# Optimization experiments

Measured on AMD Instinct MI355X. Metric: run time of the kernel, lower is better.

The kernel has to match this reference:

```python
import jax, jax.numpy as jnp
import numpy as np

C = 256        # channel
C4 = C // 4    # q/k projection dim
B, NQ, NK = 2, 8192, 8192
BN_EPS = 1e-5


def setup_inputs() -> dict:
    key = jax.random.key(0)
    ks = jax.random.split(key, 8)
    q_tensor = jax.random.normal(ks[0], (B, NQ, C), dtype=jnp.float32)
    kv_tensor = jax.random.normal(ks[1], (B, NK, C), dtype=jnp.float32)
    # 1x1 Conv1d weights == linear layers over the channel dim
    wq = jax.random.normal(ks[2], (C4, C), dtype=jnp.float32) * 0.02
    wk = jax.random.normal(ks[3], (C4, C), dtype=jnp.float32) * 0.02
    wv = jax.random.normal(ks[4], (C, C), dtype=jnp.float32) * 0.02
    wt = jax.random.normal(ks[5], (C, C), dtype=jnp.float32) * 0.02
    bt = jnp.zeros((C,), dtype=jnp.float32)
    # BatchNorm1d (eval mode): affine params + running stats
    gamma = jax.random.uniform(ks[6], (C,), dtype=jnp.float32, minval=0.5, maxval=1.5)
    beta = jax.random.normal(ks[7], (C,), dtype=jnp.float32) * 0.1
    run_mean = jnp.zeros((C,), dtype=jnp.float32)
    run_var = jnp.ones((C,), dtype=jnp.float32)
    return {"q_tensor": q_tensor, "kv_tensor": kv_tensor, "wq": wq, "wk": wk,
            "wv": wv, "wt": wt, "bt": bt, "gamma": gamma, "beta": beta,
            "run_mean": run_mean, "run_var": run_var}


def reference(q_tensor, kv_tensor, wq, wk, wv, wt, bt, gamma, beta, run_mean, run_var):
    # 1x1 conv projections (channel-last form of Conv1d on permuted input)
    x_q = jnp.einsum('bnc,dc->bnd', q_tensor, wq)    # [B, NQ, C4]
    x_k = jnp.einsum('bnc,dc->bnd', kv_tensor, wk)   # [B, NK, C4]
    x_v = jnp.einsum('bnc,dc->bnd', kv_tensor, wv)   # [B, NK, C]
    # unscaled attention: matmul -> softmax -> matmul
    energy = jnp.einsum('bqd,bkd->bqk', x_q, x_k)    # [B, NQ, NK]
    attention = jax.nn.softmax(energy, axis=-1)
    x_r = jnp.einsum('bqk,bkc->bqc', attention, x_v)  # [B, NQ, C]
    # residual difference -> trans conv -> BN (eval) -> ReLU -> residual add
    res = q_tensor - x_r
    y = jnp.einsum('bnc,dc->bnd', res, wt) + bt
    y = (y - run_mean) * jax.lax.rsqrt(run_var + BN_EPS) * gamma + beta
    return jax.nn.relu(y) + q_tensor
```

## Files before the change

kernel.cpp:

```cpp
#include <hip/hip_runtime.h>
#include <hip/hip_bf16.h>

#define DEVINL __device__ __forceinline__

typedef short bf16x8 __attribute__((ext_vector_type(8)));
typedef float f32x4  __attribute__((ext_vector_type(4)));
typedef float f32x16 __attribute__((ext_vector_type(16)));
typedef unsigned int uint2v __attribute__((ext_vector_type(2)));

struct alignas(8) S4 { short x, y, z, w; };

DEVINL short f2bf(float f) {
  __hip_bfloat16 h = __float2bfloat16(f);
  short s; __builtin_memcpy(&s, &h, 2); return s;
}
DEVINL float bf2f(short s) {
  unsigned u = ((unsigned)(unsigned short)s) << 16;
  float f; __builtin_memcpy(&f, &u, 4); return f;
}

DEVINL f32x4 mfma16(bf16x8 a, bf16x8 b, f32x4 c) {
  return __builtin_amdgcn_mfma_f32_16x16x32_bf16(a, b, c, 0, 0, 0);
}
DEVINL f32x16 mfma32(bf16x8 a, bf16x8 b, f32x16 c) {
  return __builtin_amdgcn_mfma_f32_32x32x16_bf16(a, b, c, 0, 0, 0);
}

DEVINL void gld_lds16(const void* gptr, void* lptr) {
  __builtin_amdgcn_global_load_lds(
      (const __attribute__((address_space(1))) unsigned int*)gptr,
      (__attribute__((address_space(3))) unsigned int*)lptr, 16, 0, 0);
}

#define CC 256
#define C4 64
#define BB 2
#define NQ 8192
#define NK 8192
#define NROWS (BB * NQ)
#define LOG2E 1.44269504f

__global__ void k_setup(const float* __restrict__ wq, const float* __restrict__ wk,
                        const float* __restrict__ wv, const float* __restrict__ wt,
                        const float* __restrict__ bt, const float* __restrict__ gmm,
                        const float* __restrict__ bet, const float* __restrict__ rmean,
                        const float* __restrict__ rvar,
                        short* __restrict__ wqb, short* __restrict__ wkb,
                        short* __restrict__ wvb, short* __restrict__ wtb,
                        float* __restrict__ scale, float* __restrict__ bias) {
  int i = blockIdx.x * 256 + threadIdx.x;
  if (i < C4 * CC) { wqb[i] = f2bf(wq[i] * LOG2E); wkb[i] = f2bf(wk[i]); }
  if (i < CC * CC) { wvb[i] = f2bf(wv[i]); wtb[i] = f2bf(wt[i]); }
  if (i < CC) {
    float s = gmm[i] * rsqrtf(rvar[i] + 1e-5f);
    scale[i] = s;
    bias[i]  = (bt[i] - rmean[i]) * s + bet[i];
  }
}

__global__ __launch_bounds__(256)
void k_projqk(const float* __restrict__ q, const float* __restrict__ kv,
              const short* __restrict__ wqb, const short* __restrict__ wkb,
              short* __restrict__ xq, short* __restrict__ xk) {
  const float* A; const short* W; short* O;
  const bool swz = (blockIdx.y == 1);
  if (!swz) { A = q; W = wqb; O = xq; } else { A = kv; W = wkb; O = xk; }
  const int lane = threadIdx.x & 63, w = threadIdx.x >> 6;
  const int rowbase = blockIdx.x * 64 + w * 16;
  const int lr = lane & 15, lg = lane >> 4;
  f32x4 acc[4] = {};
#pragma unroll
  for (int kf = 0; kf < 8; ++kf) {
    const float* p = A + (size_t)(rowbase + lr) * CC + kf * 32 + lg * 8;
    float4 x0 = *(const float4*)p, x1 = *(const float4*)(p + 4);
    bf16x8 a;
    a[0] = f2bf(x0.x); a[1] = f2bf(x0.y); a[2] = f2bf(x0.z); a[3] = f2bf(x0.w);
    a[4] = f2bf(x1.x); a[5] = f2bf(x1.y); a[6] = f2bf(x1.z); a[7] = f2bf(x1.w);
#pragma unroll
    for (int nf = 0; nf < 4; ++nf) {
      bf16x8 b = *(const bf16x8*)(W + (size_t)(nf * 16 + lr) * CC + kf * 32 + lg * 8);
      acc[nf] = mfma16(a, b, acc[nf]);
    }
  }
#pragma unroll
  for (int nf = 0; nf < 4; ++nf)
#pragma unroll
    for (int r = 0; r < 4; ++r) {
      int row = rowbase + lg * 4 + r;
      int d = nf * 16 + lr;
      int off = swz ? ((((d >> 3) ^ (row & 7)) << 3) + (d & 7)) : d;
      O[(size_t)row * C4 + off] = f2bf(acc[nf][r]);
    }
}

__global__ __launch_bounds__(256)
void k_projv(const float* __restrict__ kv, const short* __restrict__ wvb,
             short* __restrict__ vt) {
  const int lane = threadIdx.x & 63, w = threadIdx.x >> 6;
  const int rowbase = blockIdx.x * 64 + w * 16;
  const int cb = blockIdx.y * 128;
  const int lr = lane & 15, lg = lane >> 4;
  f32x4 acc[8] = {};
#pragma unroll
  for (int kf = 0; kf < 8; ++kf) {
    const float* p = kv + (size_t)(rowbase + lr) * CC + kf * 32 + lg * 8;
    float4 x0 = *(const float4*)p, x1 = *(const float4*)(p + 4);
    bf16x8 a;
    a[0] = f2bf(x0.x); a[1] = f2bf(x0.y); a[2] = f2bf(x0.z); a[3] = f2bf(x0.w);
    a[4] = f2bf(x1.x); a[5] = f2bf(x1.y); a[6] = f2bf(x1.z); a[7] = f2bf(x1.w);
#pragma unroll
    for (int nf = 0; nf < 8; ++nf) {
      bf16x8 b = *(const bf16x8*)(wvb + (size_t)(cb + nf * 16 + lr) * CC + kf * 32 + lg * 8);
      acc[nf] = mfma16(a, b, acc[nf]);
    }
  }
  {
    int row = rowbase + lg * 4;
    int bidx = row >> 13, kib = row & 8191;
    int tile = kib >> 6, kk = kib & 63;
#pragma unroll
    for (int nf = 0; nf < 8; ++nf) {
      int c = cb + nf * 16 + lr;
      S4 st;
      st.x = f2bf(acc[nf][0]); st.y = f2bf(acc[nf][1]);
      st.z = f2bf(acc[nf][2]); st.w = f2bf(acc[nf][3]);
      int off = (((kk >> 3) ^ (c & 7)) << 3) + (kk & 7);
      *(S4*)(vt + (((size_t)bidx * 128 + tile) * CC + c) * 64 + off) = st;
    }
  }
}

__global__ __launch_bounds__(256, 2)
void k_attn(const short* __restrict__ xq, const short* __restrict__ xk,
            const short* __restrict__ vt, float* __restrict__ xr,
            short* __restrict__ po, float* __restrict__ pl, int nsplit) {
  __shared__ char Lds[81920];
  const int tid = threadIdx.x;
  const int ln = tid & 63, w = tid >> 6;
  const int qcol = ln & 31, hi = ln >> 5;
  const int b = blockIdx.y, qt = blockIdx.x, kz = blockIdx.z;
  const int kpb = (NK / 64) / nsplit;
  const int kt0 = kz * kpb, kt1 = kt0 + kpb;

  bf16x8 qb[4];
  {
    const short* qrow = xq + (size_t)(b * NQ + qt * 128 + w * 32 + qcol) * C4;
#pragma unroll
    for (int ds = 0; ds < 4; ++ds)
      qb[ds] = *(const bf16x8*)(qrow + ds * 16 + hi * 8);
  }
  f32x16 o[8] = {};
  float lsum = 0.f;

  const char* kgbase = (const char*)(xk + (size_t)b * NK * C4);
  const char* vgbase = (const char*)(vt + (size_t)b * 128 * 16384);

  auto stage = [&](int kt, char* base) {
    const char* ks = kgbase + (size_t)kt * 8192;
    const char* vs = vgbase + (size_t)kt * 32768;
#pragma unroll
    for (int i = 0; i < 2; ++i)
      gld_lds16(ks + (w * 2 + i) * 1024 + ln * 16, base + (w * 2 + i) * 1024);
#pragma unroll
    for (int i = 0; i < 8; ++i)
      gld_lds16(vs + (w * 8 + i) * 1024 + ln * 16, base + 8192 + (w * 8 + i) * 1024);
  };

  f32x16 s[2];
  bf16x8 pb[4];

  stage(kt0, Lds);
#pragma unroll 1
  for (int t = kt0; t < kt1; ++t) {
    char* cur = Lds + ((t - kt0) & 1) * 40960;
    char* nxt = Lds + ((~(t - kt0)) & 1) * 40960;
    asm volatile("s_waitcnt vmcnt(0)" ::: "memory");
    __builtin_amdgcn_s_barrier();
    __builtin_amdgcn_sched_barrier(0);
    if (t + 1 < kt1) stage(t + 1, nxt);
    s[0] = (f32x16)0.f; s[1] = (f32x16)0.f;
    __builtin_amdgcn_s_setprio(1);
#pragma unroll
    for (int kb = 0; kb < 2; ++kb) {
      int key = kb * 32 + qcol;
#pragma unroll
      for (int ds = 0; ds < 4; ++ds) {
        int cc = ds * 2 + hi;
        bf16x8 ka = *(const bf16x8*)(cur + key * 128 + ((cc ^ (key & 7)) << 4));
        s[kb] = mfma32(ka, qb[ds], s[kb]);
      }
    }
    __builtin_amdgcn_s_setprio(0);
    float rs = 0.f;
#pragma unroll
    for (int kb = 0; kb < 2; ++kb)
#pragma unroll
      for (int r = 0; r < 16; ++r) {
        float p = __builtin_amdgcn_exp2f(s[kb][r]);
        s[kb][r] = p; rs += p;
      }
    rs += __shfl_xor(rs, 32);
    lsum += rs;
#pragma unroll
    for (int kb = 0; kb < 2; ++kb) {
      unsigned wv[4], uv[4];
#pragma unroll
      for (int j = 0; j < 4; ++j) {
        asm("v_cvt_pk_bf16_f32 %0, %1, %2"
            : "=v"(wv[j]) : "v"(s[kb][4 * j + 0]), "v"(s[kb][4 * j + 1]));
        asm("v_cvt_pk_bf16_f32 %0, %1, %2"
            : "=v"(uv[j]) : "v"(s[kb][4 * j + 2]), "v"(s[kb][4 * j + 3]));
      }
#pragma unroll
      for (int jj = 0; jj < 2; ++jj) {
        uint2v rw = __builtin_amdgcn_permlane32_swap(wv[2 * jj], wv[2 * jj + 1], false, false);
        uint2v ru = __builtin_amdgcn_permlane32_swap(uv[2 * jj], uv[2 * jj + 1], false, false);
        unsigned tmp[4] = { rw[0], ru[0], rw[1], ru[1] };
        bf16x8 t2; __builtin_memcpy(&t2, tmp, 16);
        pb[kb * 2 + jj] = t2;
      }
    }
    __builtin_amdgcn_s_setprio(1);
#pragma unroll
    for (int cb = 0; cb < 8; ++cb) {
      int c = cb * 32 + qcol;
#pragma unroll
      for (int ks = 0; ks < 4; ++ks) {
        int cc = ks * 2 + hi;
        bf16x8 va = *(const bf16x8*)(cur + 8192 + c * 128 + ((cc ^ (c & 7)) << 4));
        o[cb] = mfma32(va, pb[ks], o[cb]);
      }
    }
    __builtin_amdgcn_s_setprio(0);
  }
  __builtin_amdgcn_s_barrier();

  char* tb = Lds + w * 4096;
  const size_t rb = (size_t)b * NQ + qt * 128 + w * 32;
  if (nsplit == 1) {
    float inv = 1.f / lsum;
#pragma unroll
    for (int cb = 0; cb < 8; ++cb) {
#pragma unroll
      for (int j = 0; j < 4; ++j) {
        f32x4 v;
        v[0] = o[cb][4 * j + 0] * inv; v[1] = o[cb][4 * j + 1] * inv;
        v[2] = o[cb][4 * j + 2] * inv; v[3] = o[cb][4 * j + 3] * inv;
        *(f32x4*)(tb + qcol * 128 + (((2 * j + hi) ^ (qcol & 7)) << 4)) = v;
      }
#pragma unroll
      for (int jr = 0; jr < 4; ++jr) {
        int qr = jr * 8 + (ln >> 3), cc = ln & 7;
        f32x4 v = *(const f32x4*)(tb + qr * 128 + ((cc ^ (qr & 7)) << 4));
        *(f32x4*)(xr + (rb + qr) * CC + cb * 32 + cc * 4) = v;
      }
    }
  } else {
#pragma unroll
    for (int cb = 0; cb < 8; ++cb) {
#pragma unroll
      for (int j = 0; j < 4; ++j) {
        f32x4 v;
        v[0] = o[cb][4 * j + 0]; v[1] = o[cb][4 * j + 1];
        v[2] = o[cb][4 * j + 2]; v[3] = o[cb][4 * j + 3];
        *(f32x4*)(tb + qcol * 128 + (((2 * j + hi) ^ (qcol & 7)) << 4)) = v;
      }
#pragma unroll
      for (int jr = 0; jr < 4; ++jr) {
        int qr = jr * 8 + (ln >> 3), cc = ln & 7;
        f32x4 v = *(const f32x4*)(tb + qr * 128 + ((cc ^ (qr & 7)) << 4));
        S4 sv; sv.x = f2bf(v[0]); sv.y = f2bf(v[1]); sv.z = f2bf(v[2]); sv.w = f2bf(v[3]);
        *(S4*)(po + ((size_t)kz * NROWS + rb + qr) * CC + cb * 32 + cc * 4) = sv;
      }
    }
    if (ln < 32) {
      pl[(size_t)kz * NROWS + rb + qcol] = lsum;
    }
  }
}

__global__ __launch_bounds__(256)
void k_epilogue(const float* __restrict__ q, const float* __restrict__ xr,
                const short* __restrict__ po, const float* __restrict__ pl,
                const short* __restrict__ wtb, const float* __restrict__ scale,
                const float* __restrict__ bias, float* __restrict__ out,
                int nsplit) {
  const int lane = threadIdx.x & 63, w = threadIdx.x >> 6;
  const int rowbase = blockIdx.x * 64 + w * 16;
  const int cb = blockIdx.y * 128;
  const int lr = lane & 15, lg = lane >> 4;
  float invL = 1.f;
  if (nsplit > 1) {
    float L = 0.f;
#pragma unroll
    for (int z = 0; z < 4; ++z) L += pl[(size_t)z * NROWS + rowbase + lr];
    invL = 1.f / L;
  }
  f32x4 acc[8] = {};
#pragma unroll
  for (int kf = 0; kf < 8; ++kf) {
    size_t base = (size_t)(rowbase + lr) * CC + kf * 32 + lg * 8;
    float4 q0 = *(const float4*)(q + base), q1 = *(const float4*)(q + base + 4);
    float xv[8];
    if (nsplit > 1) {
#pragma unroll
      for (int j = 0; j < 8; ++j) xv[j] = 0.f;
#pragma unroll
      for (int z = 0; z < 4; ++z) {
        bf16x8 t = *(const bf16x8*)(po + (size_t)z * NROWS * CC + base);
#pragma unroll
        for (int j = 0; j < 8; ++j) xv[j] += bf2f(t[j]);
      }
#pragma unroll
      for (int j = 0; j < 8; ++j) xv[j] *= invL;
    } else {
      float4 r0 = *(const float4*)(xr + base), r1 = *(const float4*)(xr + base + 4);
      xv[0] = r0.x; xv[1] = r0.y; xv[2] = r0.z; xv[3] = r0.w;
      xv[4] = r1.x; xv[5] = r1.y; xv[6] = r1.z; xv[7] = r1.w;
    }
    bf16x8 a;
    a[0] = f2bf(q0.x - xv[0]); a[1] = f2bf(q0.y - xv[1]);
    a[2] = f2bf(q0.z - xv[2]); a[3] = f2bf(q0.w - xv[3]);
    a[4] = f2bf(q1.x - xv[4]); a[5] = f2bf(q1.y - xv[5]);
    a[6] = f2bf(q1.z - xv[6]); a[7] = f2bf(q1.w - xv[7]);
#pragma unroll
    for (int nf = 0; nf < 8; ++nf) {
      bf16x8 b = *(const bf16x8*)(wtb + (size_t)(cb + nf * 16 + lr) * CC + kf * 32 + lg * 8);
      acc[nf] = mfma16(a, b, acc[nf]);
    }
  }
#pragma unroll
  for (int nf = 0; nf < 8; ++nf) {
    int c = cb + nf * 16 + lr;
    float sc = scale[c], bi = bias[c];
#pragma unroll
    for (int r = 0; r < 4; ++r) {
      int row = rowbase + lg * 4 + r;
      float y = acc[nf][r] * sc + bi;
      y = fmaxf(y, 0.f) + q[(size_t)row * CC + c];
      out[(size_t)row * CC + c] = y;
    }
  }
}

extern "C" void kernel_launch(void* const* d_in, const int* in_sizes, int n_in,
                              void* d_out, int out_size, void* d_ws, size_t ws_size,
                              hipStream_t stream) {
  const float* q     = (const float*)d_in[0];
  const float* kv    = (const float*)d_in[1];
  const float* wq    = (const float*)d_in[2];
  const float* wk    = (const float*)d_in[3];
  const float* wv    = (const float*)d_in[4];
  const float* wt    = (const float*)d_in[5];
  const float* bt    = (const float*)d_in[6];
  const float* gmm   = (const float*)d_in[7];
  const float* bet   = (const float*)d_in[8];
  const float* rmean = (const float*)d_in[9];
  const float* rvar  = (const float*)d_in[10];
  float* out = (float*)d_out;
  char* ws = (char*)d_ws;

  short* wqb  = (short*)(ws + 0);
  short* wkb  = (short*)(ws + 32768);
  short* wvb  = (short*)(ws + 65536);
  short* wtb  = (short*)(ws + 196608);
  float* scale= (float*)(ws + 327680);
  float* bias = (float*)(ws + 328704);
  short* xq   = (short*)(ws + 329728);
  short* xk   = (short*)(ws + 2426880);
  short* vt   = (short*)(ws + 4524032);
  float* xr   = (float*)(ws + 12912640);
  short* po   = (short*)(ws + 29689856);
  float* pl   = (float*)(ws + 63244288);
  const size_t NEED = 63506432;
  const int nsplit = (ws_size >= NEED) ? 4 : 1;

  k_setup<<<256, 256, 0, stream>>>(wq, wk, wv, wt, bt, gmm, bet, rmean, rvar,
                                   wqb, wkb, wvb, wtb, scale, bias);
  k_projqk<<<dim3(256, 2), 256, 0, stream>>>(q, kv, wqb, wkb, xq, xk);
  k_projv<<<dim3(256, 2), 256, 0, stream>>>(kv, wvb, vt);
  k_attn<<<dim3(64, 2, nsplit), 256, 0, stream>>>(xq, xk, vt, xr, po, pl, nsplit);
  k_epilogue<<<dim3(256, 2), 256, 0, stream>>>(q, xr, po, pl, wtb, scale, bias, out, nsplit);
}
```

Baseline: 158.3 us.

## Enlarge attention tile to 256 queries with 8 waves splitting output channels

The attention kernel now runs 512 threads per block over 256 query rows. Each wave handles 64 queries (two 32-row subtiles) and half of the 256 output channels. Each K/V tile staged into LDS is therefore reused across twice as many queries, and each V fragment load feeds two MFMAs, which lowers LDS and global traffic per FLOP. In exchange, the QK^T and softmax work is duplicated across the two channel-half waves, the grid shrinks to half as many blocks, and register pressure rises under the launch bound of 512×2.

New measurement: 229.9 us. 1.45x slower.

```diff
diff --git a/kernel.cpp b/kernel.cpp
--- a/kernel.cpp
+++ b/kernel.cpp
@@ -130,7 +130,7 @@
   }
 }
 
-__global__ __launch_bounds__(256, 2)
+__global__ __launch_bounds__(512, 2)
 void k_attn(const short* __restrict__ xq, const short* __restrict__ xk,
             const short* __restrict__ vt, float* __restrict__ xr,
             short* __restrict__ po, float* __restrict__ pl, int nsplit) {
@@ -138,19 +138,22 @@
   const int tid = threadIdx.x;
   const int ln = tid & 63, w = tid >> 6;
   const int qcol = ln & 31, hi = ln >> 5;
+  const int qh = w & 3, ch = w >> 2;
   const int b = blockIdx.y, qt = blockIdx.x, kz = blockIdx.z;
   const int kpb = (NK / 64) / nsplit;
   const int kt0 = kz * kpb, kt1 = kt0 + kpb;
 
-  bf16x8 qb[4];
-  {
-    const short* qrow = xq + (size_t)(b * NQ + qt * 128 + w * 32 + qcol) * C4;
+  bf16x8 qb[2][4];
+#pragma unroll
+  for (int qj = 0; qj < 2; ++qj) {
+    const short* qrow =
+        xq + (size_t)(b * NQ + qt * 256 + qh * 64 + qj * 32 + qcol) * C4;
 #pragma unroll
     for (int ds = 0; ds < 4; ++ds)
-      qb[ds] = *(const bf16x8*)(qrow + ds * 16 + hi * 8);
-  }
-  f32x16 o[8] = {};
-  float lsum = 0.f;
+      qb[qj][ds] = *(const bf16x8*)(qrow + ds * 16 + hi * 8);
+  }
+  f32x16 o[2][4] = {};
+  float lsum0 = 0.f, lsum1 = 0.f;
 
   const char* kgbase = (const char*)(xk + (size_t)b * NK * C4);
   const char* vgbase = (const char*)(vt + (size_t)b * 128 * 16384);
@@ -158,16 +161,13 @@
   auto stage = [&](int kt, char* base) {
     const char* ks = kgbase + (size_t)kt * 8192;
     const char* vs = vgbase + (size_t)kt * 32768;
-#pragma unroll
-    for (int i = 0; i < 2; ++i)
-      gld_lds16(ks + (w * 2 + i) * 1024 + ln * 16, base + (w * 2 + i) * 1024);
-#pragma unroll
-    for (int i = 0; i < 8; ++i)
-      gld_lds16(vs + (w * 8 + i) * 1024 + ln * 16, base + 8192 + (w * 8 + i) * 1024);
+    gld_lds16(ks + w * 1024 + ln * 16, base + w * 1024);
+#pragma unroll
+    for (int i = 0; i < 4; ++i)
+      gld_lds16(vs + (w * 4 + i) * 1024 + ln * 16, base + 8192 + (w * 4 + i) * 1024);
   };
 
-  f32x16 s[2];
-  bf16x8 pb[4];
+  bf16x8 pb[2][4];
 
   stage(kt0, Lds);
 #pragma unroll 1
@@ -178,57 +178,58 @@
     __builtin_amdgcn_s_barrier();
     __builtin_amdgcn_sched_barrier(0);
     if (t + 1 < kt1) stage(t + 1, nxt);
-    s[0] = (f32x16)0.f; s[1] = (f32x16)0.f;
+#pragma unroll
+    for (int kb = 0; kb < 2; ++kb) {
+      bf16x8 ka[4];
+#pragma unroll
+      for (int ds = 0; ds < 4; ++ds) {
+        int key = kb * 32 + qcol, cc = ds * 2 + hi;
+        ka[ds] = *(const bf16x8*)(cur + key * 128 + ((cc ^ (key & 7)) << 4));
+      }
+#pragma unroll
+      for (int qj = 0; qj < 2; ++qj) {
+        f32x16 s = (f32x16)0.f;
+        __builtin_amdgcn_s_setprio(1);
+#pragma unroll
+        for (int ds = 0; ds < 4; ++ds)
+          s = mfma32(ka[ds], qb[qj][ds], s);
+        __builtin_amdgcn_s_setprio(0);
+        float rs = 0.f;
+#pragma unroll
+        for (int r = 0; r < 16; ++r) {
+          float p = __builtin_amdgcn_exp2f(s[r]);
+          s[r] = p; rs += p;
+        }
+        rs += __shfl_xor(rs, 32);
+        if (qj == 0) lsum0 += rs; else lsum1 += rs;
+        unsigned wv[4], uv[4];
+#pragma unroll
+        for (int j = 0; j < 4; ++j) {
+          asm("v_cvt_pk_bf16_f32 %0, %1, %2"
+              : "=v"(wv[j]) : "v"(s[4 * j + 0]), "v"(s[4 * j + 1]));
+          asm("v_cvt_pk_bf16_f32 %0, %1, %2"
+              : "=v"(uv[j]) : "v"(s[4 * j + 2]), "v"(s[4 * j + 3]));
+        }
+#pragma unroll
+        for (int jj = 0; jj < 2; ++jj) {
+          uint2v rw = __builtin_amdgcn_permlane32_swap(wv[2 * jj], wv[2 * jj + 1], false, false);
+          uint2v ru = __builtin_amdgcn_permlane32_swap(uv[2 * jj], uv[2 * jj + 1], false, false);
+          unsigned tmp[4] = { rw[0], ru[0], rw[1], ru[1] };
+          bf16x8 t2; __builtin_memcpy(&t2, tmp, 16);
+          pb[qj][kb * 2 + jj] = t2;
+        }
+      }
+    }
     __builtin_amdgcn_s_setprio(1);
 #pragma unroll
-    for (int kb = 0; kb < 2; ++kb) {
-      int key = kb * 32 + qcol;
-#pragma unroll
-      for (int ds = 0; ds < 4; ++ds) {
-        int cc = ds * 2 + hi;
-        bf16x8 ka = *(const bf16x8*)(cur + key * 128 + ((cc ^ (key & 7)) << 4));
-        s[kb] = mfma32(ka, qb[ds], s[kb]);
-      }
-    }
-    __builtin_amdgcn_s_setprio(0);
-    float rs = 0.f;
-#pragma unroll
-    for (int kb = 0; kb < 2; ++kb)
-#pragma unroll
-      for (int r = 0; r < 16; ++r) {
-        float p = __builtin_amdgcn_exp2f(s[kb][r]);
-        s[kb][r] = p; rs += p;
-      }
-    rs += __shfl_xor(rs, 32);
-    lsum += rs;
-#pragma unroll
-    for (int kb = 0; kb < 2; ++kb) {
-      unsigned wv[4], uv[4];
-#pragma unroll
-      for (int j = 0; j < 4; ++j) {
-        asm("v_cvt_pk_bf16_f32 %0, %1, %2"
-            : "=v"(wv[j]) : "v"(s[kb][4 * j + 0]), "v"(s[kb][4 * j + 1]));
-        asm("v_cvt_pk_bf16_f32 %0, %1, %2"
-            : "=v"(uv[j]) : "v"(s[kb][4 * j + 2]), "v"(s[kb][4 * j + 3]));
-      }
-#pragma unroll
-      for (int jj = 0; jj < 2; ++jj) {
-        uint2v rw = __builtin_amdgcn_permlane32_swap(wv[2 * jj], wv[2 * jj + 1], false, false);
-        uint2v ru = __builtin_amdgcn_permlane32_swap(uv[2 * jj], uv[2 * jj + 1], false, false);
-        unsigned tmp[4] = { rw[0], ru[0], rw[1], ru[1] };
-        bf16x8 t2; __builtin_memcpy(&t2, tmp, 16);
-        pb[kb * 2 + jj] = t2;
-      }
-    }
-    __builtin_amdgcn_s_setprio(1);
-#pragma unroll
-    for (int cb = 0; cb < 8; ++cb) {
-      int c = cb * 32 + qcol;
+    for (int cb = 0; cb < 4; ++cb) {
+      int c = ch * 128 + cb * 32 + qcol;
 #pragma unroll
       for (int ks = 0; ks < 4; ++ks) {
         int cc = ks * 2 + hi;
         bf16x8 va = *(const bf16x8*)(cur + 8192 + c * 128 + ((cc ^ (c & 7)) << 4));
-        o[cb] = mfma32(va, pb[ks], o[cb]);
+        o[0][cb] = mfma32(va, pb[0][ks], o[0][cb]);
+        o[1][cb] = mfma32(va, pb[1][ks], o[1][cb]);
       }
     }
     __builtin_amdgcn_s_setprio(0);
@@ -236,46 +237,50 @@
   __builtin_amdgcn_s_barrier();
 
   char* tb = Lds + w * 4096;
-  const size_t rb = (size_t)b * NQ + qt * 128 + w * 32;
-  if (nsplit == 1) {
-    float inv = 1.f / lsum;
-#pragma unroll
-    for (int cb = 0; cb < 8; ++cb) {
-#pragma unroll
-      for (int j = 0; j < 4; ++j) {
-        f32x4 v;
-        v[0] = o[cb][4 * j + 0] * inv; v[1] = o[cb][4 * j + 1] * inv;
-        v[2] = o[cb][4 * j + 2] * inv; v[3] = o[cb][4 * j + 3] * inv;
-        *(f32x4*)(tb + qcol * 128 + (((2 * j + hi) ^ (qcol & 7)) << 4)) = v;
-      }
-#pragma unroll
-      for (int jr = 0; jr < 4; ++jr) {
-        int qr = jr * 8 + (ln >> 3), cc = ln & 7;
-        f32x4 v = *(const f32x4*)(tb + qr * 128 + ((cc ^ (qr & 7)) << 4));
-        *(f32x4*)(xr + (rb + qr) * CC + cb * 32 + cc * 4) = v;
-      }
-    }
-  } else {
-#pragma unroll
-    for (int cb = 0; cb < 8; ++cb) {
-#pragma unroll
-      for (int j = 0; j < 4; ++j) {
-        f32x4 v;
-        v[0] = o[cb][4 * j + 0]; v[1] = o[cb][4 * j + 1];
-        v[2] = o[cb][4 * j + 2]; v[3] = o[cb][4 * j + 3];
-        *(f32x4*)(tb + qcol * 128 + (((2 * j + hi) ^ (qcol & 7)) << 4)) = v;
-      }
-#pragma unroll
-      for (int jr = 0; jr < 4; ++jr) {
-        int qr = jr * 8 + (ln >> 3), cc = ln & 7;
-        f32x4 v = *(const f32x4*)(tb + qr * 128 + ((cc ^ (qr & 7)) << 4));
-        S4 sv; sv.x = f2bf(v[0]); sv.y = f2bf(v[1]); sv.z = f2bf(v[2]); sv.w = f2bf(v[3]);
-        *(S4*)(po + ((size_t)kz * NROWS + rb + qr) * CC + cb * 32 + cc * 4) = sv;
-      }
-    }
-    if (ln < 32) {
-      pl[(size_t)kz * NROWS + rb + qcol] = lsum;
-    }
+  const size_t rb = (size_t)b * NQ + qt * 256 + qh * 64;
+  const int cbase = ch * 128;
+  float inv0 = 1.f / lsum0, inv1 = 1.f / lsum1;
+#pragma unroll
+  for (int qj = 0; qj < 2; ++qj) {
+    float inv = qj ? inv1 : inv0;
+#pragma unroll
+    for (int cb = 0; cb < 4; ++cb) {
+      if (nsplit == 1) {
+#pragma unroll
+        for (int j = 0; j < 4; ++j) {
+          f32x4 v;
+          v[0] = o[qj][cb][4 * j + 0] * inv; v[1] = o[qj][cb][4 * j + 1] * inv;
+          v[2] = o[qj][cb][4 * j + 2] * inv; v[3] = o[qj][cb][4 * j + 3] * inv;
+          *(f32x4*)(tb + qcol * 128 + (((2 * j + hi) ^ (qcol & 7)) << 4)) = v;
+        }
+#pragma unroll
+        for (int jr = 0; jr < 4; ++jr) {
+          int qr = jr * 8 + (ln >> 3), cc2 = ln & 7;
+          f32x4 v = *(const f32x4*)(tb + qr * 128 + ((cc2 ^ (qr & 7)) << 4));
+          *(f32x4*)(xr + (rb + qj * 32 + qr) * CC + cbase + cb * 32 + cc2 * 4) = v;
+        }
+      } else {
+#pragma unroll
+        for (int j = 0; j < 4; ++j) {
+          f32x4 v;
+          v[0] = o[qj][cb][4 * j + 0]; v[1] = o[qj][cb][4 * j + 1];
+          v[2] = o[qj][cb][4 * j + 2]; v[3] = o[qj][cb][4 * j + 3];
+          *(f32x4*)(tb + qcol * 128 + (((2 * j + hi) ^ (qcol & 7)) << 4)) = v;
+        }
+#pragma unroll
+        for (int jr = 0; jr < 4; ++jr) {
+          int qr = jr * 8 + (ln >> 3), cc2 = ln & 7;
+          f32x4 v = *(const f32x4*)(tb + qr * 128 + ((cc2 ^ (qr & 7)) << 4));
+          S4 sv; sv.x = f2bf(v[0]); sv.y = f2bf(v[1]); sv.z = f2bf(v[2]); sv.w = f2bf(v[3]);
+          *(S4*)(po + ((size_t)kz * NROWS + rb + qj * 32 + qr) * CC +
+                 cbase + cb * 32 + cc2 * 4) = sv;
+        }
+      }
+    }
+  }
+  if (nsplit > 1 && ch == 0 && ln < 32) {
+    pl[(size_t)kz * NROWS + rb + qcol]      = lsum0;
+    pl[(size_t)kz * NROWS + rb + 32 + qcol] = lsum1;
   }
 }
 
@@ -379,6 +384,6 @@
                                    wqb, wkb, wvb, wtb, scale, bias);
   k_projqk<<<dim3(256, 2), 256, 0, stream>>>(q, kv, wqb, wkb, xq, xk);
   k_projv<<<dim3(256, 2), 256, 0, stream>>>(kv, wvb, vt);
-  k_attn<<<dim3(64, 2, nsplit), 256, 0, stream>>>(xq, xk, vt, xr, po, pl, nsplit);
+  k_attn<<<dim3(32, 2, nsplit), 512, 0, stream>>>(xq, xk, vt, xr, po, pl, nsplit);
   k_epilogue<<<dim3(256, 2), 256, 0, stream>>>(q, xr, po, pl, wtb, scale, bias, out, nsplit);
 }
```
